# Kernel tuning notes

Hardware: AMD Instinct MI355X
Metric: run time of the kernel (lower is better)

## Reference

```python
import jax, jax.numpy as jnp
import numpy as np

# Spiking time schedule: B_n = (1+0.5)*X_n = 1500 per spiking layer (X_n=1000),
# chained via set_params: layer k has t_min = 1500*k, t_max = 1500*(k+1).
B_N = 1500.0


def _region_idx(H, W):
    # 0=center, 1=TL, 2=top, 3=TR, 4=right, 5=BR, 6=bottom, 7=BL, 8=left
    r = np.zeros((H, W), np.int32)
    r[0, :] = 2; r[-1, :] = 6; r[:, 0] = 8; r[:, -1] = 4
    r[0, 0] = 1; r[0, -1] = 3; r[-1, -1] = 5; r[-1, 0] = 7
    return jnp.asarray(r)


def _im2col3(x, t_min):
    # x: [B,H,W,C] -> patches [B,H,W,9*C]; 'same' pad with value t_min
    B, H, W, C = x.shape
    xp = jnp.pad(x, ((0, 0), (1, 1), (1, 1), (0, 0)), constant_values=t_min)
    cols = [xp[:, dy:dy + H, dx:dx + W, :] for dy in range(3) for dx in range(3)]
    return jnp.concatenate(cols, axis=-1)


def _spiking_conv(x, Wk, D, t_min, t_max):
    # ti = (tj - t_min) @ W + (t_max - t_min - D_region) + t_min, clamped at t_max
    p = _im2col3(x, t_min)                       # [B,H,W,9C]
    lin = jnp.einsum('bhwk,kf->bhwf', p - t_min, Wk)
    Dmap = D[_region_idx(x.shape[1], x.shape[2])]  # [H,W,F] border-aware thresholds
    return jnp.minimum(lin + (t_max - Dmap), t_max)


def _spiking_dense(x, Wk, D, t_min, t_max):
    return jnp.minimum((x - t_min) @ Wk + (t_max - D), t_max)


def _pool2(x):
    B, H, W, C = x.shape
    return x.reshape(B, H // 2, 2, W // 2, 2, C).max(axis=(2, 4))


def _forward(x, Wc1, Dc1, Wc2, Dc2, Wc3, Dc3, Wc4, Dc4, Wd1, Dd1, Wout, Dout):
    x = _spiking_conv(x, Wc1, Dc1, 0.0, 1500.0)
    x = _spiking_conv(x, Wc2, Dc2, 1500.0, 3000.0)
    x = _pool2(x)
    x = _spiking_conv(x, Wc3, Dc3, 3000.0, 4500.0)
    x = _spiking_conv(x, Wc4, Dc4, 4500.0, 6000.0)
    x = _pool2(x)
    x = x.reshape(x.shape[0], -1)                 # [B, 16*16*128]
    x = _spiking_dense(x, Wd1, Dd1, 6000.0, 7500.0)
    # output layer: alpha*(t_min - t_min_prev) + (t_min - tj)@W == D_i + (t_min - tj)@W
    return Dout + (7500.0 - x) @ Wout


def setup_inputs() -> dict:
    key = jax.random.key(0)
    ks = jax.random.split(key, 14)
    B, H, C0 = 32, 64, 1

    def w(k, fan_in, fan_out):
        return (jax.random.normal(k, (fan_in, fan_out), jnp.float32)
                / np.float32(np.sqrt(fan_in)))

    def d(k, shape):
        return jax.random.uniform(k, shape, jnp.float32) * 10.0

    return {
        'x': jax.random.uniform(ks[0], (B, H, H, C0), jnp.float32),
        'Wc1': w(ks[1], 9 * C0, 64),    'Dc1': d(ks[2], (9, 64)),
        'Wc2': w(ks[3], 9 * 64, 64),    'Dc2': d(ks[4], (9, 64)),
        'Wc3': w(ks[5], 9 * 64, 128),   'Dc3': d(ks[6], (9, 128)),
        'Wc4': w(ks[7], 9 * 128, 128),  'Dc4': d(ks[8], (9, 128)),
        'Wd1': w(ks[9], 16 * 16 * 128, 256), 'Dd1': d(ks[10], (256,)),
        'Wout': w(ks[11], 256, 10),     'Dout': d(ks[12], (10,)),
    }


def reference(x, Wc1, Dc1, Wc2, Dc2, Wc3, Dc3, Wc4, Dc4, Wd1, Dd1, Wout, Dout):
    return _forward(x, Wc1, Dc1, Wc2, Dc2, Wc3, Dc3, Wc4, Dc4, Wd1, Dd1, Wout, Dout)
```

## Files before the change

kernel.cpp:

```cpp
#include <hip/hip_runtime.h>
#include <hip/hip_bf16.h>

#define DEVINL __device__ __forceinline__

typedef __attribute__((ext_vector_type(8)))  short short8;
typedef __attribute__((ext_vector_type(4)))  float float4v;

DEVINL float bf2f(unsigned short u) { return __uint_as_float(((unsigned)u) << 16); }
DEVINL unsigned short f2bf(float f) {
  unsigned u = __float_as_uint(f);
  unsigned r = u + 0x7FFFu + ((u >> 16) & 1u);
  return (unsigned short)(r >> 16);
}

DEVINL int region_of(int h, int w, int n) {
  if (h == 0)     return (w == 0) ? 1 : ((w == n-1) ? 3 : 2);
  if (h == n-1)   return (w == 0) ? 7 : ((w == n-1) ? 5 : 6);
  return (w == 0) ? 8 : ((w == n-1) ? 4 : 0);
}

__global__ void sentinel_k(float* out, float v) {
  int t = blockIdx.x*64 + threadIdx.x;
  if (t < 320) out[t] = v;
}

__global__ void wtrans_all(const float* __restrict__ W2, const float* __restrict__ W3,
                           const float* __restrict__ W4,
                           unsigned short* __restrict__ T2, unsigned short* __restrict__ T3,
                           unsigned short* __restrict__ T4)
{
  int y = blockIdx.y;
  const float* W = (y == 0) ? W2 : (y == 1) ? W3 : W4;
  unsigned short* T = (y == 0) ? T2 : (y == 1) ? T3 : T4;
  int Ksteps = (y == 2) ? 36 : 18;
  int NT = (y == 0) ? 4 : 8;
  int F  = (y == 0) ? 64 : 128;
  int i = blockIdx.x*256 + threadIdx.x;
  if (i >= Ksteps*NT*64) return;
  int lane = i & 63, nt = (i >> 6) % NT, kstep = i / (64*NT);
  int f = nt*16 + (lane & 15);
  int kbase = kstep*32 + (lane >> 4)*8;
  unsigned short v[8];
  #pragma unroll
  for (int j = 0; j < 8; j++) v[j] = f2bf(W[(kbase + j)*F + f]);
  ushort4* q = (ushort4*)&T[(size_t)i * 8];
  q[0] = make_ushort4(v[0], v[1], v[2], v[3]);
  q[1] = make_ushort4(v[4], v[5], v[6], v[7]);
}

__global__ __launch_bounds__(256) void conv1_k(const float* __restrict__ x,
    const float* __restrict__ Wf, const float* __restrict__ Df,
    unsigned short* __restrict__ out)
{
  int h = blockIdx.x, b = blockIdx.y, t = threadIdx.x;
  __shared__ float a[3][66];
  for (int idx = t; idx < 3*66; idx += 256) {
    int dy = idx / 66, wcol = idx % 66;
    int hh = h + dy - 1, w = wcol - 1;
    float v = 0.f;
    if (hh >= 0 && hh < 64 && w >= 0 && w < 64)
      v = x[(b*64 + hh)*64 + w];
    a[dy][wcol] = v;
  }
  __syncthreads();
  int f = t & 63, wq = t >> 6;
  float wk[9];
  #pragma unroll
  for (int k = 0; k < 9; k++) wk[k] = Wf[k*64 + f];
  for (int wi = 0; wi < 16; wi++) {
    int w = wq*16 + wi;
    float acc = 0.f;
    #pragma unroll
    for (int dy = 0; dy < 3; dy++)
      #pragma unroll
      for (int dx = 0; dx < 3; dx++)
        acc += a[dy][w+dx] * wk[dy*3+dx];
    int r = region_of(h, w, 64);
    out[((b*64 + h)*64 + w)*64 + f] = f2bf(fminf(acc - Df[r*64 + f], 0.f));
  }
}

template<int C, int F, int N, bool POOL, int WSM>
__global__ __launch_bounds__(256) void conv_mfma(
    const unsigned short* __restrict__ U, const unsigned short* __restrict__ Wt,
    const float* __restrict__ Df, unsigned short* __restrict__ out)
{
  constexpr int RC   = POOL ? 2 : 1;
  constexpr int ROWS = RC + 2;
  constexpr int Cpad = C + 8;
  constexpr int NT = F / 16;
  constexpr int MT = N / 16;
  constexpr int WSN = 4 / WSM;
  constexpr int MW = MT / WSM;
  constexpr int NW = NT / WSN;

  __shared__ __align__(16) unsigned short lds[ROWS*(N+2)*Cpad];

  int b = blockIdx.y, hp = blockIdx.x, t = threadIdx.x;
  int h0 = hp * RC;

  const int stage16 = ROWS*(N+2)*(C/8);
  #pragma unroll 4
  for (int i = t; i < stage16; i += 256) {
    int c8 = i % (C/8), wc = (i/(C/8)) % (N+2), r = i/((C/8)*(N+2));
    int hh = h0 - 1 + r, w = wc - 1;
    float4 v = make_float4(0.f,0.f,0.f,0.f);
    if (hh >= 0 && hh < N && w >= 0 && w < N)
      v = *(const float4*)&U[(((size_t)b*N + hh)*N + w)*C + c8*8];
    *(float4*)&lds[(r*(N+2) + wc)*Cpad + c8*8] = v;
  }
  __syncthreads();

  int lane = t & 63, wave = t >> 6;
  int wm = wave / WSN, wn = wave % WSN;
  int quad = lane >> 4, lm = lane & 15;

  union ABu { float4 f4; short8 v; };

  float4v acc[RC][MW][NW];
  #pragma unroll
  for (int hi = 0; hi < RC; hi++)
    #pragma unroll
    for (int m = 0; m < MW; m++)
      #pragma unroll
      for (int n = 0; n < NW; n++)
        acc[hi][m][n] = (float4v){0.f, 0.f, 0.f, 0.f};

  #pragma unroll
  for (int dy = 0; dy < 3; dy++)
  #pragma unroll
  for (int dx = 0; dx < 3; dx++)
  #pragma unroll
  for (int c0 = 0; c0 < C; c0 += 32) {
    int kstep = (dy*3 + dx)*(C/32) + (c0 >> 5);
    ABu bfr[NW];
    #pragma unroll
    for (int n = 0; n < NW; n++)
      bfr[n].f4 = *(const float4*)&Wt[(size_t)((kstep*NT + wn*NW + n)*64 + lane)*8];
    #pragma unroll
    for (int hi = 0; hi < RC; hi++) {
      ABu afr[MW];
      #pragma unroll
      for (int m = 0; m < MW; m++)
        afr[m].f4 = *(const float4*)&lds[((hi+dy)*(N+2) + ((wm*MW + m)*16 + lm + dx))*Cpad + c0 + quad*8];
      #pragma unroll
      for (int n = 0; n < NW; n++)
        #pragma unroll
        for (int m = 0; m < MW; m++)
          acc[hi][m][n] = __builtin_amdgcn_mfma_f32_16x16x32_bf16(afr[m].v, bfr[n].v, acc[hi][m][n], 0, 0, 0);
    }
  }

  if constexpr (POOL) {
    constexpr int M2 = N/2;
    #pragma unroll
    for (int m = 0; m < MW; m++)
      #pragma unroll
      for (int n = 0; n < NW; n++) {
        int mm = wm*MW + m;
        int f = (wn*NW + n)*16 + lm;
        #pragma unroll
        for (int rp = 0; rp < 2; rp++) {
          float mx = -1e30f;
          #pragma unroll
          for (int hi = 0; hi < 2; hi++)
            #pragma unroll
            for (int rr = 0; rr < 2; rr++) {
              int h = h0 + hi, w = mm*16 + quad*4 + 2*rp + rr;
              float v = fminf(acc[hi][m][n][2*rp+rr] - Df[region_of(h, w, N)*F + f], 0.f);
              mx = fmaxf(mx, v);
            }
          int wp = mm*8 + quad*2 + rp;
          out[(((size_t)b*M2 + hp)*M2 + wp)*F + f] = f2bf(mx);
        }
      }
  } else {
    int h = h0;
    #pragma unroll
    for (int m = 0; m < MW; m++)
      #pragma unroll
      for (int n = 0; n < NW; n++) {
        int mm = wm*MW + m;
        int f = (wn*NW + n)*16 + lm;
        #pragma unroll
        for (int r = 0; r < 4; r++) {
          int w = mm*16 + quad*4 + r;
          int reg = region_of(h, w, N);
          float v = fminf(acc[0][m][n][r] - Df[reg*F + f], 0.f);
          out[(((size_t)b*N + h)*N + w)*F + f] = f2bf(v);
        }
      }
  }
}

__global__ __launch_bounds__(256) void dense_k(const unsigned short* __restrict__ act,
    const float* __restrict__ W, float* __restrict__ part)
{
  int blk = blockIdx.x, t = threadIdx.x;
  int kblk = blk >> 1, fh = blk & 1;
  int k0 = kblk * 128;
  __shared__ float a[128][36];
  for (int idx = t; idx < 32*128; idx += 256) {
    int bb = idx >> 7, kc = idx & 127;
    a[kc][bb] = bf2f(act[(size_t)bb*32768 + k0 + kc]);
  }
  __syncthreads();
  int f0 = fh*128 + (t & 31)*4, b0 = (t >> 5)*4;
  float acc[4][4] = {};
  #pragma unroll 8
  for (int kc = 0; kc < 128; kc++) {
    float4 wv = *(const float4*)&W[(size_t)(k0 + kc)*256 + f0];
    float4 av = *(const float4*)&a[kc][b0];
    const float* avp = (const float*)&av;
    #pragma unroll
    for (int bb = 0; bb < 4; bb++) {
      float avx = avp[bb];
      acc[bb][0] += avx * wv.x;
      acc[bb][1] += avx * wv.y;
      acc[bb][2] += avx * wv.z;
      acc[bb][3] += avx * wv.w;
    }
  }
  #pragma unroll
  for (int bb = 0; bb < 4; bb++) {
    float4 v = make_float4(acc[bb][0], acc[bb][1], acc[bb][2], acc[bb][3]);
    *(float4*)&part[(size_t)kblk*8192 + (b0+bb)*256 + f0] = v;
  }
}

__global__ void reduce_k(const float* __restrict__ part, const float* __restrict__ Dd,
                         float* __restrict__ ud)
{
  int i = blockIdx.x*256 + threadIdx.x;
  float s = 0.f;
  #pragma unroll 16
  for (int blk = 0; blk < 256; blk++) s += part[(size_t)blk*8192 + i];
  ud[i] = fminf(s - Dd[i & 255], 0.f);
}

__global__ void final_k(const float* __restrict__ ud, const float* __restrict__ Wo,
                        const float* __restrict__ Do, float* __restrict__ out)
{
  int t = blockIdx.x*64 + threadIdx.x;
  if (t >= 320) return;
  int b = t / 10, o = t % 10;
  float acc = 0.f;
  #pragma unroll 8
  for (int f = 0; f < 256; f++) acc += ud[b*256 + f] * Wo[f*10 + o];
  out[t] = Do[o] - acc;
}

extern "C" void kernel_launch(void* const* d_in, const int* in_sizes, int n_in,
                              void* d_out, int out_size, void* d_ws, size_t ws_size,
                              hipStream_t stream)
{
  float* outp = (float*)d_out;

  if (n_in != 13) { sentinel_k<<<5, 64, 0, stream>>>(outp, 200.f); return; }
  const int exp_sz[13] = {131072, 576, 576, 36864, 576, 73728, 1152,
                          147456, 1152, 8388608, 256, 2560, 10};
  for (int i = 0; i < 13; i++)
    if (in_sizes[i] != exp_sz[i]) {
      sentinel_k<<<5, 64, 0, stream>>>(outp, 1000.f + 100.f*i); return;
    }
  if (ws_size < (37u << 20)) { sentinel_k<<<5, 64, 0, stream>>>(outp, 500.f); return; }

  char* wsb = (char*)d_ws;
  const float* x    = (const float*)d_in[0];
  const float* Wc1  = (const float*)d_in[1];
  const float* Dc1  = (const float*)d_in[2];
  const float* Wc2  = (const float*)d_in[3];
  const float* Dc2  = (const float*)d_in[4];
  const float* Wc3  = (const float*)d_in[5];
  const float* Dc3  = (const float*)d_in[6];
  const float* Wc4  = (const float*)d_in[7];
  const float* Dc4  = (const float*)d_in[8];
  const float* Wd1  = (const float*)d_in[9];
  const float* Dd1  = (const float*)d_in[10];
  const float* Wout = (const float*)d_in[11];
  const float* Dout = (const float*)d_in[12];

  float* ud = (float*)wsb;
  unsigned short* Wt2 = (unsigned short*)(wsb + (1u << 20));
  unsigned short* Wt3 = (unsigned short*)(wsb + (1u << 20) + 262144);
  unsigned short* Wt4 = (unsigned short*)(wsb + (1u << 20) + 524288);
  unsigned short* U1 = (unsigned short*)(wsb + (2u  << 20));
  unsigned short* P2 = (unsigned short*)(wsb + (19u << 20));
  unsigned short* U3 = (unsigned short*)(wsb + (2u  << 20));
  unsigned short* P4 = (unsigned short*)(wsb + (19u << 20));
  float* part        = (float*)(wsb + (2u  << 20));

  wtrans_all<<<dim3(72, 3), 256, 0, stream>>>(Wc2, Wc3, Wc4, Wt2, Wt3, Wt4);
  conv1_k<<<dim3(64, 32), 256, 0, stream>>>(x, Wc1, Dc1, U1);
  conv_mfma<64, 64, 64, true, 2><<<dim3(32, 32), 256, 0, stream>>>(U1, Wt2, Dc2, P2);
  conv_mfma<64, 128, 32, false, 1><<<dim3(32, 32), 256, 0, stream>>>(P2, Wt3, Dc3, U3);
  conv_mfma<128, 128, 32, true, 1><<<dim3(16, 32), 256, 0, stream>>>(U3, Wt4, Dc4, P4);
  dense_k<<<512, 256, 0, stream>>>(P4, Wd1, part);
  reduce_k<<<32, 256, 0, stream>>>(part, Dd1, ud);
  final_k<<<5, 64, 0, stream>>>(ud, Wout, Dout, outp);
}
```

Measured before the change: 180.9 us.

## Fuse conv1 into conv2+pool MFMA kernel and merge reduce with final layer

Conv1 is now computed on the fly into shared memory as a 4-row halo tile (bf16). The conv2 MFMA with 2x2 max-pool then reads that tile directly, so the full-resolution U1 activation is never written to or read from global memory. The dense-reduce and output-layer kernels are merged into one block per batch item that does a shared-memory reduction and a wave shuffle dot product, removing a launch. In exchange, conv1 work is recomputed for halo rows, and each block now uses more shared memory and registers, which may lower occupancy.

```diff
diff --git a/kernel.cpp b/kernel.cpp
--- a/kernel.cpp
+++ b/kernel.cpp
@@ -48,36 +48,125 @@
   q[1] = make_ushort4(v[4], v[5], v[6], v[7]);
 }
 
-__global__ __launch_bounds__(256) void conv1_k(const float* __restrict__ x,
-    const float* __restrict__ Wf, const float* __restrict__ Df,
+__global__ __launch_bounds__(256) void conv12_k(const float* __restrict__ x,
+    const float* __restrict__ Wf1, const float* __restrict__ Df1,
+    const unsigned short* __restrict__ Wt, const float* __restrict__ Df2,
     unsigned short* __restrict__ out)
 {
-  int h = blockIdx.x, b = blockIdx.y, t = threadIdx.x;
-  __shared__ float a[3][66];
-  for (int idx = t; idx < 3*66; idx += 256) {
-    int dy = idx / 66, wcol = idx % 66;
-    int hh = h + dy - 1, w = wcol - 1;
+  constexpr int Cpad = 72;
+  __shared__ __align__(16) unsigned short u[4*66*Cpad];
+  __shared__ float xs[6][66];
+
+  int b = blockIdx.y, hp = blockIdx.x, t = threadIdx.x;
+  int h0 = hp * 2;
+
+  for (int idx = t; idx < 6*66; idx += 256) {
+    int r = idx / 66, wc = idx % 66;
+    int hh = h0 - 2 + r, w = wc - 1;
     float v = 0.f;
-    if (hh >= 0 && hh < 64 && w >= 0 && w < 64)
-      v = x[(b*64 + hh)*64 + w];
-    a[dy][wcol] = v;
-  }
-  __syncthreads();
-  int f = t & 63, wq = t >> 6;
-  float wk[9];
-  #pragma unroll
-  for (int k = 0; k < 9; k++) wk[k] = Wf[k*64 + f];
-  for (int wi = 0; wi < 16; wi++) {
-    int w = wq*16 + wi;
-    float acc = 0.f;
-    #pragma unroll
-    for (int dy = 0; dy < 3; dy++)
-      #pragma unroll
-      for (int dx = 0; dx < 3; dx++)
-        acc += a[dy][w+dx] * wk[dy*3+dx];
-    int r = region_of(h, w, 64);
-    out[((b*64 + h)*64 + w)*64 + f] = f2bf(fminf(acc - Df[r*64 + f], 0.f));
-  }
+    if (hh >= 0 && hh < 64 && w >= 0 && w < 64) v = x[(b*64 + hh)*64 + w];
+    xs[r][wc] = v;
+  }
+  __syncthreads();
+
+  {
+    int f2 = (t & 31) * 2, g = t >> 5;
+    int r = g & 3, wh = g >> 2;
+    int hh = h0 - 1 + r;
+    bool valid = (hh >= 0 && hh < 64);
+    float wka[9], wkb[9];
+    #pragma unroll
+    for (int k = 0; k < 9; k++) {
+      wka[k] = Wf1[k*64 + f2];
+      wkb[k] = Wf1[k*64 + f2 + 1];
+    }
+    int w0 = wh * 32;
+    float cA0 = xs[r+0][w0], cA1 = xs[r+1][w0], cA2 = xs[r+2][w0];
+    float cB0 = xs[r+0][w0+1], cB1 = xs[r+1][w0+1], cB2 = xs[r+2][w0+1];
+    for (int wi = 0; wi < 32; wi++) {
+      int w = w0 + wi;
+      float cC0 = xs[r+0][w+2], cC1 = xs[r+1][w+2], cC2 = xs[r+2][w+2];
+      float aa = cA0*wka[0] + cB0*wka[1] + cC0*wka[2]
+               + cA1*wka[3] + cB1*wka[4] + cC1*wka[5]
+               + cA2*wka[6] + cB2*wka[7] + cC2*wka[8];
+      float ab = cA0*wkb[0] + cB0*wkb[1] + cC0*wkb[2]
+               + cA1*wkb[3] + cB1*wkb[4] + cC1*wkb[5]
+               + cA2*wkb[6] + cB2*wkb[7] + cC2*wkb[8];
+      float va = 0.f, vb = 0.f;
+      if (valid) {
+        int reg = region_of(hh, w, 64);
+        va = fminf(aa - Df1[reg*64 + f2],     0.f);
+        vb = fminf(ab - Df1[reg*64 + f2 + 1], 0.f);
+      }
+      unsigned pk = (unsigned)f2bf(va) | ((unsigned)f2bf(vb) << 16);
+      *(unsigned*)&u[(r*66 + (w+1))*Cpad + f2] = pk;
+      cA0 = cB0; cB0 = cC0; cA1 = cB1; cB1 = cC1; cA2 = cB2; cB2 = cC2;
+    }
+    *(unsigned*)&u[(r*66 + (wh ? 65 : 0))*Cpad + f2] = 0u;
+  }
+  __syncthreads();
+
+  int lane = t & 63, wave = t >> 6;
+  int wm = wave >> 1, wn = wave & 1;
+  int quad = lane >> 4, lm = lane & 15;
+
+  union ABu { float4 f4; short8 v; };
+
+  float4v acc[2][2][2];
+  #pragma unroll
+  for (int hi = 0; hi < 2; hi++)
+    #pragma unroll
+    for (int m = 0; m < 2; m++)
+      #pragma unroll
+      for (int n = 0; n < 2; n++)
+        acc[hi][m][n] = (float4v){0.f, 0.f, 0.f, 0.f};
+
+  #pragma unroll
+  for (int dy = 0; dy < 3; dy++)
+  #pragma unroll
+  for (int dx = 0; dx < 3; dx++)
+  #pragma unroll
+  for (int c0 = 0; c0 < 64; c0 += 32) {
+    int kstep = (dy*3 + dx)*2 + (c0 >> 5);
+    ABu bfr[2];
+    #pragma unroll
+    for (int n = 0; n < 2; n++)
+      bfr[n].f4 = *(const float4*)&Wt[(size_t)((kstep*4 + wn*2 + n)*64 + lane)*8];
+    #pragma unroll
+    for (int hi = 0; hi < 2; hi++) {
+      ABu afr[2];
+      #pragma unroll
+      for (int m = 0; m < 2; m++)
+        afr[m].f4 = *(const float4*)&u[((hi+dy)*66 + ((wm*2 + m)*16 + lm + dx))*Cpad + c0 + quad*8];
+      #pragma unroll
+      for (int n = 0; n < 2; n++)
+        #pragma unroll
+        for (int m = 0; m < 2; m++)
+          acc[hi][m][n] = __builtin_amdgcn_mfma_f32_16x16x32_bf16(afr[m].v, bfr[n].v, acc[hi][m][n], 0, 0, 0);
+    }
+  }
+
+  #pragma unroll
+  for (int m = 0; m < 2; m++)
+    #pragma unroll
+    for (int n = 0; n < 2; n++) {
+      int mm = wm*2 + m;
+      int f = (wn*2 + n)*16 + lm;
+      #pragma unroll
+      for (int rp = 0; rp < 2; rp++) {
+        float mx = -1e30f;
+        #pragma unroll
+        for (int hi = 0; hi < 2; hi++)
+          #pragma unroll
+          for (int rr = 0; rr < 2; rr++) {
+            int h = h0 + hi, w = mm*16 + quad*4 + 2*rp + rr;
+            float v = fminf(acc[hi][m][n][2*rp+rr] - Df2[region_of(h, w, 64)*64 + f], 0.f);
+            mx = fmaxf(mx, v);
+          }
+        int wp = mm*8 + quad*2 + rp;
+        out[(((size_t)b*32 + hp)*32 + wp)*64 + f] = f2bf(mx);
+      }
+    }
 }
 
 template<int C, int F, int N, bool POOL, int WSM>
@@ -228,26 +317,39 @@
   }
 }
 
-__global__ void reduce_k(const float* __restrict__ part, const float* __restrict__ Dd,
-                         float* __restrict__ ud)
-{
-  int i = blockIdx.x*256 + threadIdx.x;
+__global__ __launch_bounds__(1024) void redfin_k(const float* __restrict__ part,
+    const float* __restrict__ Dd, const float* __restrict__ Wo,
+    const float* __restrict__ Do, float* __restrict__ out)
+{
+  int b = blockIdx.x, t = threadIdx.x;
+  int f = t & 255, kq = t >> 8;
   float s = 0.f;
   #pragma unroll 16
-  for (int blk = 0; blk < 256; blk++) s += part[(size_t)blk*8192 + i];
-  ud[i] = fminf(s - Dd[i & 255], 0.f);
-}
-
-__global__ void final_k(const float* __restrict__ ud, const float* __restrict__ Wo,
-                        const float* __restrict__ Do, float* __restrict__ out)
-{
-  int t = blockIdx.x*64 + threadIdx.x;
-  if (t >= 320) return;
-  int b = t / 10, o = t % 10;
-  float acc = 0.f;
-  #pragma unroll 8
-  for (int f = 0; f < 256; f++) acc += ud[b*256 + f] * Wo[f*10 + o];
-  out[t] = Do[o] - acc;
+  for (int blk = kq*64; blk < kq*64 + 64; blk++)
+    s += part[(size_t)blk*8192 + b*256 + f];
+  __shared__ float red[4][256];
+  red[kq][f] = s;
+  __syncthreads();
+  __shared__ float ud[256];
+  if (t < 256) {
+    float v = red[0][t] + red[1][t] + red[2][t] + red[3][t];
+    ud[t] = fminf(v - Dd[t], 0.f);
+  }
+  __syncthreads();
+  int lane = t & 63, wave = t >> 6;
+  if (wave < 4) {
+    for (int o = wave; o < 10; o += 4) {
+      float acc = 0.f;
+      #pragma unroll
+      for (int j = 0; j < 4; j++) {
+        int ff = j*64 + lane;
+        acc += ud[ff] * Wo[ff*10 + o];
+      }
+      #pragma unroll
+      for (int off = 32; off; off >>= 1) acc += __shfl_down(acc, off, 64);
+      if (lane == 0) out[b*10 + o] = Do[o] - acc;
+    }
+  }
 }
 
 extern "C" void kernel_launch(void* const* d_in, const int* in_sizes, int n_in,
@@ -280,22 +382,18 @@
   const float* Wout = (const float*)d_in[11];
   const float* Dout = (const float*)d_in[12];
 
-  float* ud = (float*)wsb;
   unsigned short* Wt2 = (unsigned short*)(wsb + (1u << 20));
   unsigned short* Wt3 = (unsigned short*)(wsb + (1u << 20) + 262144);
   unsigned short* Wt4 = (unsigned short*)(wsb + (1u << 20) + 524288);
-  unsigned short* U1 = (unsigned short*)(wsb + (2u  << 20));
   unsigned short* P2 = (unsigned short*)(wsb + (19u << 20));
   unsigned short* U3 = (unsigned short*)(wsb + (2u  << 20));
   unsigned short* P4 = (unsigned short*)(wsb + (19u << 20));
   float* part        = (float*)(wsb + (2u  << 20));
 
   wtrans_all<<<dim3(72, 3), 256, 0, stream>>>(Wc2, Wc3, Wc4, Wt2, Wt3, Wt4);
-  conv1_k<<<dim3(64, 32), 256, 0, stream>>>(x, Wc1, Dc1, U1);
-  conv_mfma<64, 64, 64, true, 2><<<dim3(32, 32), 256, 0, stream>>>(U1, Wt2, Dc2, P2);
+  conv12_k<<<dim3(32, 32), 256, 0, stream>>>(x, Wc1, Dc1, Wt2, Dc2, P2);
   conv_mfma<64, 128, 32, false, 1><<<dim3(32, 32), 256, 0, stream>>>(P2, Wt3, Dc3, U3);
   conv_mfma<128, 128, 32, true, 1><<<dim3(16, 32), 256, 0, stream>>>(U3, Wt4, Dc4, P4);
   dense_k<<<512, 256, 0, stream>>>(P4, Wd1, part);
-  reduce_k<<<32, 256, 0, stream>>>(part, Dd1, ud);
-  final_k<<<5, 64, 0, stream>>>(ud, Wout, Dout, outp);
-}
+  redfin_k<<<32, 1024, 0, stream>>>(part, Dd1, Wout, Dout, outp);
+}
```

Result: faster. 163.0 us (-9.9%).
